# Optimization experiments

Measured on AMD Instinct MI355X. Metric: run time of the kernel, lower is better.

## Reference

```python
import math
import jax, jax.numpy as jnp
import numpy as np

NQ = 4   # n_qubits
NL = 2   # n_layers
H = 16   # num_heads


def _apply_gate(state, gate, q, batched):
    """Apply a 1-qubit gate on wire q to batched state [N, 2**NQ]."""
    n = state.shape[0]
    left, right = 2 ** q, 2 ** (NQ - 1 - q)
    s = state.reshape(n, left, 2, right)
    eq = 'nab,nlbr->nlar' if batched else 'ab,nlbr->nlar'
    return jnp.einsum(eq, gate, s).reshape(n, 2 ** NQ)


def _rot(phi, theta, omega):
    """PennyLane Rot(phi, theta, omega) = RZ(omega) RY(theta) RZ(phi), 2x2 unitary."""
    c = jnp.cos(theta / 2).astype(jnp.complex64)
    s = jnp.sin(theta / 2).astype(jnp.complex64)
    ep = jnp.exp(-0.5j * (phi + omega).astype(jnp.complex64))
    em = jnp.exp(0.5j * (phi - omega).astype(jnp.complex64))
    m00 = ep * c
    m01 = -em * s
    m10 = jnp.conj(em) * s
    m11 = jnp.conj(ep) * c
    return jnp.stack([jnp.stack([m00, m01]), jnp.stack([m10, m11])])


def _cnot01(state):
    """CNOT with control wire 0, target wire 1 on [N, 16]."""
    n = state.shape[0]
    s = state.reshape(n, 2, 2, 2 ** (NQ - 2))
    s = jnp.stack([s[:, 0], s[:, 1, ::-1]], axis=1)
    return s.reshape(n, 2 ** NQ)


def _quantum_block(inputs, params):
    """Analytic state-vector simulation of the PennyLane circuit.

    inputs: [N, NQ] rotation angles (AngleEmbedding, default RX).
    params: [NL, NQ, 3] Rot parameters.
    Returns [N, NQ] Pauli-Z expectation values.
    """
    n = inputs.shape[0]
    state = jnp.zeros((n, 2 ** NQ), jnp.complex64).at[:, 0].set(1.0)
    # AngleEmbedding: RX(inputs[:, q]) on wire q
    for q in range(NQ):
        a = inputs[:, q] * 0.5
        c = jnp.cos(a).astype(jnp.complex64)
        s = (-1j) * jnp.sin(a).astype(jnp.complex64)
        gate = jnp.stack([jnp.stack([c, s], -1), jnp.stack([s, c], -1)], -2)  # [N,2,2]
        state = _apply_gate(state, gate, q, batched=True)
    # Variational layers
    for l in range(NL):
        for q in range(NQ):
            g = _rot(params[l, q, 0], params[l, q, 1], params[l, q, 2])
            state = _apply_gate(state, g, q, batched=False)
        state = _cnot01(state)
    probs = (jnp.abs(state) ** 2).reshape(n, 2, 2, 2, 2)
    z = jnp.array([1.0, -1.0], probs.dtype)
    letters = 'abcd'
    evs = [jnp.einsum(f'nabcd,{letters[i]}->n', probs, z) for i in range(NQ)]
    return jnp.stack(evs, axis=-1)


def reference(x, params, w_q, w_k, w_v, w_o):
    B, S, E = x.shape
    dk = E // H

    def proj(w):
        return (x @ w.T).reshape(B, S, H, dk).transpose(0, 2, 1, 3)  # [B,H,S,dk]

    q, k, v = proj(w_q), proj(w_k), proj(w_v)

    def inject(t):
        ang = t[..., :NQ].reshape(-1, NQ)
        ev = _quantum_block(ang, params).reshape(B, H, S, NQ).astype(t.dtype)
        return t.at[..., :NQ].set(ev)

    q, k, v = inject(q), inject(k), inject(v)
    scores = jnp.einsum('bhqd,bhkd->bhqk', q, k) / math.sqrt(dk)
    attn = jax.nn.softmax(scores, axis=-1)
    out = jnp.einsum('bhqk,bhkd->bhqd', attn, v)
    out = out.transpose(0, 2, 1, 3).reshape(B, S, E)
    return out @ w_o.T


def setup_inputs() -> dict:
    key = jax.random.key(0)
    ks = jax.random.split(key, 6)
    B, S, E = 2, 2048, 1024
    scale = 1.0 / math.sqrt(E)
    return {
        'x': jax.random.normal(ks[0], (B, S, E), jnp.float32),
        'params': jax.random.normal(ks[1], (NL, NQ, 3), jnp.float32),
        'w_q': jax.random.normal(ks[2], (E, E), jnp.float32) * scale,
        'w_k': jax.random.normal(ks[3], (E, E), jnp.float32) * scale,
        'w_v': jax.random.normal(ks[4], (E, E), jnp.float32) * scale,
        'w_o': jax.random.normal(ks[5], (E, E), jnp.float32) * scale,
    }
```

## Files before the change

kernel.cpp:

```cpp
#include <hip/hip_runtime.h>
#include <math.h>

#define BATCH 2
#define S_LEN 2048
#define E_DIM 1024
#define NHEAD 16
#define DK 64
#define NROWS (BATCH * S_LEN)

typedef _Float16 f16x8 __attribute__((ext_vector_type(8)));
typedef _Float16 f16x4 __attribute__((ext_vector_type(4)));
typedef float    f32x4 __attribute__((ext_vector_type(4)));

__device__ __forceinline__ void glds16(_Float16* lds, const _Float16* g) {
    __builtin_amdgcn_global_load_lds(
        (const __attribute__((address_space(1))) unsigned int*)g,
        (__attribute__((address_space(3))) unsigned int*)lds,
        16, 0, 0);
}

__global__ __launch_bounds__(256) void conv_all(
    const float* __restrict__ x,  const float* __restrict__ wq,
    const float* __restrict__ wk, const float* __restrict__ wv,
    const float* __restrict__ wo,
    _Float16* __restrict__ xh,  _Float16* __restrict__ wqh,
    _Float16* __restrict__ wkh, _Float16* __restrict__ wvh,
    _Float16* __restrict__ woh) {
    const int id = blockIdx.x;
    const float* src; _Float16* dst; int lid;
    if (id < 4096)      { src = x;  dst = xh;  lid = id; }
    else if (id < 5120) { src = wq; dst = wqh; lid = id - 4096; }
    else if (id < 6144) { src = wk; dst = wkh; lid = id - 5120; }
    else if (id < 7168) { src = wv; dst = wvh; lid = id - 6144; }
    else                { src = wo; dst = woh; lid = id - 7168; }
    const int i = lid * 256 + threadIdx.x;
    float4 v = ((const float4*)src)[i];
    f16x4 h;
    h[0] = (_Float16)v.x; h[1] = (_Float16)v.y;
    h[2] = (_Float16)v.z; h[3] = (_Float16)v.w;
    ((f16x4*)dst)[i] = h;
}

__device__ __forceinline__ void gemm_body(const _Float16* __restrict__ X,
                                          const _Float16* __restrict__ W,
                                          void* __restrict__ dstv, int mode,
                                          _Float16* smem) {
    _Float16* Xs = smem;
    _Float16* Ws = smem + 128 * 64;

    const int tid  = threadIdx.x;
    const int lane = tid & 63;
    const int w    = tid >> 6;
    const int wy = w >> 1, wx = w & 1;
    const int l15 = lane & 15, quad = lane >> 4;
    const int sw  = l15 & 7;
    const int m0 = blockIdx.y * 128, c0 = blockIdx.x * 128;

    const int lrow = lane >> 3;
    const int gcol = ((lane & 7) ^ lrow) * 8;
    const _Float16* xg = X + (size_t)(m0 + w * 32 + lrow) * E_DIM + gcol;
    const _Float16* wg = W + (size_t)(c0 + w * 32 + lrow) * E_DIM + gcol;
    _Float16* xls = Xs + (w * 32) * 64;
    _Float16* wls = Ws + (w * 32) * 64;

    f32x4 acc[4][4];
#pragma unroll
    for (int i = 0; i < 4; ++i)
#pragma unroll
        for (int j = 0; j < 4; ++j) acc[i][j] = 0.f;

    for (int k0 = 0; k0 < E_DIM; k0 += 64) {
        __syncthreads();
#pragma unroll
        for (int c = 0; c < 4; ++c)
            glds16(xls + c * 512, xg + (size_t)c * 8 * E_DIM + k0);
#pragma unroll
        for (int c = 0; c < 4; ++c)
            glds16(wls + c * 512, wg + (size_t)c * 8 * E_DIM + k0);
        __syncthreads();

#pragma unroll
        for (int ks = 0; ks < 2; ++ks) {
            f16x8 af[4], bf[4];
#pragma unroll
            for (int i = 0; i < 4; ++i) {
                const int pc = ((ks * 4 + quad) ^ sw) * 8;
                af[i] = *(const f16x8*)&Xs[(wy * 64 + i * 16 + l15) * 64 + pc];
                bf[i] = *(const f16x8*)&Ws[(wx * 64 + i * 16 + l15) * 64 + pc];
            }
#pragma unroll
            for (int i = 0; i < 4; ++i)
#pragma unroll
                for (int j = 0; j < 4; ++j)
                    acc[i][j] = __builtin_amdgcn_mfma_f32_16x16x32_f16(af[i], bf[j], acc[i][j], 0, 0, 0);
        }
    }

    if (mode == 2) {
        __syncthreads();
        _Float16* Ct = smem;
#pragma unroll
        for (int i = 0; i < 4; ++i)
#pragma unroll
            for (int j = 0; j < 4; ++j) {
                const int col  = wx * 64 + j * 16 + l15;
                const int rowb = wy * 64 + i * 16 + quad * 4;
                f16x4 pk;
#pragma unroll
                for (int r = 0; r < 4; ++r) pk[r] = (_Float16)acc[i][j][r];
                *(f16x4*)&Ct[col * 136 + rowb] = pk;
            }
        __syncthreads();
        const int b  = m0 >> 11;
        const int s0 = m0 & 2047;
#pragma unroll
        for (int it = 0; it < 8; ++it) {
            const int c   = it * 256 + tid;
            const int col = c >> 4;
            const int rc  = c & 15;
            f16x8 v = *(const f16x8*)&Ct[col * 136 + rc * 8];
            const int e = c0 + col, h = e >> 6, d = e & 63;
            *(f16x8*)((_Float16*)dstv + ((size_t)((b * NHEAD + h) * DK + d)) * S_LEN + s0 + rc * 8) = v;
        }
        return;
    }

#pragma unroll
    for (int i = 0; i < 4; ++i)
#pragma unroll
        for (int j = 0; j < 4; ++j)
#pragma unroll
            for (int r = 0; r < 4; ++r) {
                const int row = m0 + wy * 64 + i * 16 + quad * 4 + r;
                const int col = c0 + wx * 64 + j * 16 + l15;
                const int b = row >> 11, s = row & 2047;
                const int h = col >> 6,  d = col & 63;
                ((_Float16*)dstv)[(((size_t)(b * NHEAD + h) * S_LEN + s) * DK) + d] =
                    (_Float16)acc[i][j][r];
            }
}

__global__ __launch_bounds__(256, 3) void gemm_qkv(
    const _Float16* __restrict__ X,
    const _Float16* __restrict__ WQ, const _Float16* __restrict__ WK,
    const _Float16* __restrict__ WV,
    _Float16* __restrict__ Qh, _Float16* __restrict__ Kh,
    _Float16* __restrict__ VTh) {
    __shared__ __align__(16) _Float16 smem[128 * 136];
    const int z = blockIdx.z;
    const _Float16* W = (z == 0) ? WQ : (z == 1) ? WK : WV;
    void* dst = (z == 0) ? (void*)Qh : (z == 1) ? (void*)Kh : (void*)VTh;
    gemm_body(X, W, dst, (z == 2) ? 2 : 1, smem);
}

__global__ __launch_bounds__(256, 2) void gemm_out2(const _Float16* __restrict__ X,
                                                    const _Float16* __restrict__ W,
                                                    float* __restrict__ dst) {
    __shared__ __align__(16) _Float16 smem[128 * 64 + 64 * 64];
    _Float16* Xs = smem;
    _Float16* Ws = smem + 128 * 64;

    const int tid  = threadIdx.x;
    const int lane = tid & 63;
    const int w    = tid >> 6;
    const int wy = w >> 1, wx = w & 1;
    const int l15 = lane & 15, quad = lane >> 4;
    const int sw  = l15 & 7;
    const int m0 = blockIdx.y * 128, c0 = blockIdx.x * 64;

    const int lrow = lane >> 3;
    const int gcol = ((lane & 7) ^ lrow) * 8;
    const _Float16* xg = X + (size_t)(m0 + w * 32 + lrow) * E_DIM + gcol;
    const _Float16* wg = W + (size_t)(c0 + w * 16 + lrow) * E_DIM + gcol;
    _Float16* xls = Xs + (w * 32) * 64;
    _Float16* wls = Ws + (w * 16) * 64;

    f32x4 acc[4][2];
#pragma unroll
    for (int i = 0; i < 4; ++i)
#pragma unroll
        for (int j = 0; j < 2; ++j) acc[i][j] = 0.f;

    for (int k0 = 0; k0 < E_DIM; k0 += 64) {
        __syncthreads();
#pragma unroll
        for (int c = 0; c < 4; ++c)
            glds16(xls + c * 512, xg + (size_t)c * 8 * E_DIM + k0);
#pragma unroll
        for (int c = 0; c < 2; ++c)
            glds16(wls + c * 512, wg + (size_t)c * 8 * E_DIM + k0);
        __syncthreads();

#pragma unroll
        for (int ks = 0; ks < 2; ++ks) {
            f16x8 af[4], bf[2];
#pragma unroll
            for (int i = 0; i < 4; ++i) {
                const int pc = ((ks * 4 + quad) ^ sw) * 8;
                af[i] = *(const f16x8*)&Xs[(wy * 64 + i * 16 + l15) * 64 + pc];
            }
#pragma unroll
            for (int j = 0; j < 2; ++j) {
                const int pc = ((ks * 4 + quad) ^ sw) * 8;
                bf[j] = *(const f16x8*)&Ws[(wx * 32 + j * 16 + l15) * 64 + pc];
            }
#pragma unroll
            for (int i = 0; i < 4; ++i)
#pragma unroll
                for (int j = 0; j < 2; ++j)
                    acc[i][j] = __builtin_amdgcn_mfma_f32_16x16x32_f16(af[i], bf[j], acc[i][j], 0, 0, 0);
        }
    }

#pragma unroll
    for (int i = 0; i < 4; ++i)
#pragma unroll
        for (int j = 0; j < 2; ++j)
#pragma unroll
            for (int r = 0; r < 4; ++r) {
                const int row = m0 + wy * 64 + i * 16 + quad * 4 + r;
                const int col = c0 + wx * 32 + j * 16 + l15;
                dst[(size_t)row * E_DIM + col] = acc[i][j][r];
            }
}

__device__ __forceinline__ void apply_gate(float ar[16], float ai[16], int stride,
                                           float g00r, float g00i, float g01r, float g01i,
                                           float g10r, float g10i, float g11r, float g11i) {
#pragma unroll
    for (int i0 = 0; i0 < 16; ++i0) {
        if (i0 & stride) continue;
        const int i1 = i0 + stride;
        const float s0r = ar[i0], s0i = ai[i0];
        const float s1r = ar[i1], s1i = ai[i1];
        ar[i0] = g00r * s0r - g00i * s0i + g01r * s1r - g01i * s1i;
        ai[i0] = g00r * s0i + g00i * s0r + g01r * s1i + g01i * s1r;
        ar[i1] = g10r * s0r - g10i * s0i + g11r * s1r - g11i * s1i;
        ai[i1] = g10r * s0i + g10i * s0r + g11r * s1i + g11i * s1r;
    }
}

__global__ __launch_bounds__(256) void quantum_inject(_Float16* __restrict__ Q,
                                                      _Float16* __restrict__ K,
                                                      _Float16* __restrict__ VT,
                                                      const float* __restrict__ params) {
    const int id = blockIdx.x * 256 + threadIdx.x;
    const int which = id >> 16;
    const int rem = id & 65535;

    float angv[4];
    _Float16* qkbase = nullptr;
    _Float16* vbase  = nullptr;
    if (which == 2) {
        const int bh = rem >> 11, s = rem & 2047;
        vbase = VT + ((size_t)bh * DK) * S_LEN + s;
#pragma unroll
        for (int d = 0; d < 4; ++d) angv[d] = (float)vbase[(size_t)d * S_LEN];
    } else {
        qkbase = (which == 0 ? Q : K) + (size_t)rem * DK;
        const f16x4 a4 = *(const f16x4*)qkbase;
#pragma unroll
        for (int d = 0; d < 4; ++d) angv[d] = (float)a4[d];
    }

    float ar[16], ai[16];
#pragma unroll
    for (int i = 0; i < 16; ++i) { ar[i] = 0.f; ai[i] = 0.f; }
    ar[0] = 1.f;

#pragma unroll
    for (int q = 0; q < 4; ++q) {
        float sh, ch;
        sincosf(0.5f * angv[q], &sh, &ch);
        apply_gate(ar, ai, 8 >> q, ch, 0.f, 0.f, -sh, 0.f, -sh, ch, 0.f);
    }

#pragma unroll
    for (int l = 0; l < 2; ++l) {
#pragma unroll
        for (int q = 0; q < 4; ++q) {
            const float* pp = params + (l * 4 + q) * 3;
            const float phi = pp[0], th = pp[1], om = pp[2];
            float st, ct, sa, ca, sb, cb;
            sincosf(0.5f * th, &st, &ct);
            sincosf(0.5f * (phi + om), &sa, &ca);
            sincosf(0.5f * (phi - om), &sb, &cb);
            apply_gate(ar, ai, 8 >> q,
                       ct * ca, -ct * sa,
                       -st * cb, -st * sb,
                       st * cb, -st * sb,
                       ct * ca, ct * sa);
        }
#pragma unroll
        for (int r = 0; r < 4; ++r) {
            float tr = ar[8 + r], ti = ai[8 + r];
            ar[8 + r] = ar[12 + r]; ai[8 + r] = ai[12 + r];
            ar[12 + r] = tr;        ai[12 + r] = ti;
        }
    }

    float ev[4] = {0.f, 0.f, 0.f, 0.f};
#pragma unroll
    for (int i = 0; i < 16; ++i) {
        const float p = ar[i] * ar[i] + ai[i] * ai[i];
        ev[0] += (i & 8) ? -p : p;
        ev[1] += (i & 4) ? -p : p;
        ev[2] += (i & 2) ? -p : p;
        ev[3] += (i & 1) ? -p : p;
    }
    if (which == 2) {
#pragma unroll
        for (int d = 0; d < 4; ++d) vbase[(size_t)d * S_LEN] = (_Float16)ev[d];
    } else {
        f16x4 o;
#pragma unroll
        for (int d = 0; d < 4; ++d) o[d] = (_Float16)ev[d];
        *(f16x4*)qkbase = o;
    }
}

__global__ __launch_bounds__(256, 3) void attn7(const _Float16* __restrict__ Q,
                                                const _Float16* __restrict__ K,
                                                const _Float16* __restrict__ VT,
                                                _Float16* __restrict__ ctx) {
    __shared__ __align__(16) _Float16 KVs[2][2][64 * 64];

    const int tid = threadIdx.x, lane = tid & 63, w = tid >> 6;
    const int l15 = lane & 15, quad = lane >> 4;
    const int sw  = l15 & 7;
    const int bh = blockIdx.y;
    const int qbase = blockIdx.x * 128 + w * 32;

    const _Float16* Qb = Q  + (size_t)bh * S_LEN * DK;
    const _Float16* Kb = K  + (size_t)bh * S_LEN * DK;
    const _Float16* Vb = VT + (size_t)bh * DK * S_LEN;

    const int lrow = lane >> 3;
    const int gcol = ((lane & 7) ^ lrow) * 8;
    const int sr0  = 32 * (w >> 1) + 8 * (lrow >> 2) + 4 * (w & 1) + (lrow & 3);
    const _Float16* kg = Kb + (size_t)sr0 * DK + gcol;
    const _Float16* vg = Vb + (size_t)(w * 16 + lrow) * S_LEN + gcol;

    f16x8 bf[2][2];
#pragma unroll
    for (int qn = 0; qn < 2; ++qn)
#pragma unroll
        for (int ks = 0; ks < 2; ++ks)
            bf[qn][ks] = *(const f16x8*)(Qb + (size_t)(qbase + qn * 16 + l15) * DK + ks * 32 + quad * 8);

    f32x4 oacc[4][2];
#pragma unroll
    for (int dt = 0; dt < 4; ++dt)
#pragma unroll
        for (int qn = 0; qn < 2; ++qn) oacc[dt][qn] = 0.f;
    float lpart[2] = {0.f, 0.f};

#pragma unroll
    for (int c = 0; c < 2; ++c) {
        glds16(&KVs[0][0][(w * 16 + c * 8) * 64], kg + (size_t)(c * 16) * DK);
        glds16(&KVs[0][1][(w * 16 + c * 8) * 64], vg + (size_t)(c * 8) * S_LEN);
    }
    __syncthreads();

    for (int t = 0; t < S_LEN / 64; ++t) {
        const int buf = t & 1;
        if (t < S_LEN / 64 - 1) {
            const int kt = (t + 1) * 64;
#pragma unroll
            for (int c = 0; c < 2; ++c) {
                glds16(&KVs[buf ^ 1][0][(w * 16 + c * 8) * 64],
                       kg + (size_t)(kt + c * 16) * DK);
                glds16(&KVs[buf ^ 1][1][(w * 16 + c * 8) * 64],
                       vg + (size_t)(c * 8) * S_LEN + kt);
            }
        }

        f16x8 af[4][2], vt[4][2];
#pragma unroll
        for (int kc = 0; kc < 4; ++kc)
#pragma unroll
            for (int ks = 0; ks < 2; ++ks)
                af[kc][ks] = *(const f16x8*)&KVs[buf][0][(kc * 16 + l15) * 64 + ((ks * 4 + quad) ^ sw) * 8];
#pragma unroll
        for (int dt = 0; dt < 4; ++dt)
#pragma unroll
            for (int kh = 0; kh < 2; ++kh)
                vt[dt][kh] = *(const f16x8*)&KVs[buf][1][(dt * 16 + l15) * 64 + ((kh * 4 + quad) ^ sw) * 8];

        f16x4 pk4s[4][2];
#pragma unroll
        for (int kc = 0; kc < 4; ++kc)
#pragma unroll
            for (int qn = 0; qn < 2; ++qn) {
                f32x4 st = 0.f;
                st = __builtin_amdgcn_mfma_f32_16x16x32_f16(af[kc][0], bf[qn][0], st, 0, 0, 0);
                st = __builtin_amdgcn_mfma_f32_16x16x32_f16(af[kc][1], bf[qn][1], st, 0, 0, 0);
                float ps = 0.f;
                f16x4 pk;
#pragma unroll
                for (int r = 0; r < 4; ++r) {
                    const float p = __builtin_amdgcn_exp2f(
                        fmaf(st[r], 0.18033688011f, -4.32808512267f));
                    ps += p;
                    pk[r] = (_Float16)p;
                }
                lpart[qn] += ps;
                pk4s[kc][qn] = pk;
            }

#pragma unroll
        for (int dt = 0; dt < 4; ++dt)
#pragma unroll
            for (int qn = 0; qn < 2; ++qn)
#pragma unroll
                for (int kh = 0; kh < 2; ++kh) {
                    const f16x8 pb = __builtin_shufflevector(
                        pk4s[2 * kh][qn], pk4s[2 * kh + 1][qn],
                        0, 1, 2, 3, 4, 5, 6, 7);
                    oacc[dt][qn] = __builtin_amdgcn_mfma_f32_16x16x32_f16(
                        vt[dt][kh], pb, oacc[dt][qn], 0, 0, 0);
                }

        __syncthreads();
    }

    float inv[2];
#pragma unroll
    for (int qn = 0; qn < 2; ++qn) {
        float l = lpart[qn];
        l += __shfl_xor(l, 16);
        l += __shfl_xor(l, 32);
        inv[qn] = 1.f / l;
    }

    _Float16* ep = &KVs[0][0][0] + w * (32 * 72);
#pragma unroll
    for (int dt = 0; dt < 4; ++dt)
#pragma unroll
        for (int qn = 0; qn < 2; ++qn) {
            f16x4 ov;
#pragma unroll
            for (int r = 0; r < 4; ++r) ov[r] = (_Float16)(oacc[dt][qn][r] * inv[qn]);
            *(f16x4*)&ep[(qn * 16 + l15) * 72 + dt * 16 + quad * 4] = ov;
        }

    const int b = bh >> 4, h = bh & 15;
#pragma unroll
    for (int i = 0; i < 4; ++i) {
        const int c = i * 64 + lane;
        const int row = c >> 3, c8 = c & 7;
        f16x8 v = *(const f16x8*)&ep[row * 72 + c8 * 8];
        *(f16x8*)(ctx + (size_t)(b * S_LEN + qbase + row) * E_DIM + h * DK + c8 * 8) = v;
    }
}

extern "C" void kernel_launch(void* const* d_in, const int* in_sizes, int n_in,
                              void* d_out, int out_size, void* d_ws, size_t ws_size,
                              hipStream_t stream) {
    const float* x      = (const float*)d_in[0];
    const float* params = (const float*)d_in[1];
    const float* w_q    = (const float*)d_in[2];
    const float* w_k    = (const float*)d_in[3];
    const float* w_v    = (const float*)d_in[4];
    const float* w_o    = (const float*)d_in[5];
    float* out = (float*)d_out;

    const size_t TENS = (size_t)NROWS * E_DIM;
    const size_t WEL  = (size_t)E_DIM * E_DIM;
    _Float16* xh  = (_Float16*)d_ws;
    _Float16* wqh = xh  + TENS;
    _Float16* wkh = wqh + WEL;
    _Float16* wvh = wkh + WEL;
    _Float16* woh = wvh + WEL;
    _Float16* Qh  = woh + WEL;
    _Float16* Kh  = Qh  + TENS;
    _Float16* VTh = Kh  + TENS;
    _Float16* CTXh= VTh + TENS;

    dim3 blk(256);

    conv_all<<<dim3(8192), blk, 0, stream>>>(x, w_q, w_k, w_v, w_o,
                                             xh, wqh, wkh, wvh, woh);

    gemm_qkv<<<dim3(E_DIM / 128, NROWS / 128, 3), blk, 0, stream>>>(
        xh, wqh, wkh, wvh, Qh, Kh, VTh);

    quantum_inject<<<dim3(768), blk, 0, stream>>>(Qh, Kh, VTh, params);

    attn7<<<dim3(S_LEN / 128, BATCH * NHEAD), blk, 0, stream>>>(Qh, Kh, VTh, CTXh);

    gemm_out2<<<dim3(E_DIM / 64, NROWS / 128), blk, 0, stream>>>(CTXh, woh, out);
}
```

Measured before the change: 197.9 us.

## Double-buffer LDS tiles in QKV and output GEMMs to overlap loads with MFMA

After: 190.3 us. -3.9%, faster.

```diff
diff --git a/kernel.cpp b/kernel.cpp
--- a/kernel.cpp
+++ b/kernel.cpp
@@ -45,9 +45,6 @@
                                           const _Float16* __restrict__ W,
                                           void* __restrict__ dstv, int mode,
                                           _Float16* smem) {
-    _Float16* Xs = smem;
-    _Float16* Ws = smem + 128 * 64;
-
     const int tid  = threadIdx.x;
     const int lane = tid & 63;
     const int w    = tid >> 6;
@@ -60,8 +57,7 @@
     const int gcol = ((lane & 7) ^ lrow) * 8;
     const _Float16* xg = X + (size_t)(m0 + w * 32 + lrow) * E_DIM + gcol;
     const _Float16* wg = W + (size_t)(c0 + w * 32 + lrow) * E_DIM + gcol;
-    _Float16* xls = Xs + (w * 32) * 64;
-    _Float16* wls = Ws + (w * 32) * 64;
+    const int woff = (w * 32) * 64;
 
     f32x4 acc[4][4];
 #pragma unroll
@@ -69,15 +65,26 @@
 #pragma unroll
         for (int j = 0; j < 4; ++j) acc[i][j] = 0.f;
 
-    for (int k0 = 0; k0 < E_DIM; k0 += 64) {
-        __syncthreads();
-#pragma unroll
-        for (int c = 0; c < 4; ++c)
-            glds16(xls + c * 512, xg + (size_t)c * 8 * E_DIM + k0);
-#pragma unroll
-        for (int c = 0; c < 4; ++c)
-            glds16(wls + c * 512, wg + (size_t)c * 8 * E_DIM + k0);
-        __syncthreads();
+#pragma unroll
+    for (int c = 0; c < 4; ++c) {
+        glds16(smem + woff + c * 512,        xg + (size_t)c * 8 * E_DIM);
+        glds16(smem + 8192 + woff + c * 512, wg + (size_t)c * 8 * E_DIM);
+    }
+    __syncthreads();
+
+    for (int t = 0; t < E_DIM / 64; ++t) {
+        const int buf = t & 1;
+        _Float16* Xs = smem + buf * 16384;
+        _Float16* Ws = Xs + 8192;
+        if (t < E_DIM / 64 - 1) {
+            _Float16* Xn = smem + (buf ^ 1) * 16384;
+            const int k0 = (t + 1) * 64;
+#pragma unroll
+            for (int c = 0; c < 4; ++c) {
+                glds16(Xn + woff + c * 512,        xg + (size_t)c * 8 * E_DIM + k0);
+                glds16(Xn + 8192 + woff + c * 512, wg + (size_t)c * 8 * E_DIM + k0);
+            }
+        }
 
 #pragma unroll
         for (int ks = 0; ks < 2; ++ks) {
@@ -94,10 +101,10 @@
                 for (int j = 0; j < 4; ++j)
                     acc[i][j] = __builtin_amdgcn_mfma_f32_16x16x32_f16(af[i], bf[j], acc[i][j], 0, 0, 0);
         }
+        __syncthreads();
     }
 
     if (mode == 2) {
-        __syncthreads();
         _Float16* Ct = smem;
 #pragma unroll
         for (int i = 0; i < 4; ++i)
@@ -140,25 +147,23 @@
             }
 }
 
-__global__ __launch_bounds__(256, 3) void gemm_qkv(
+__global__ __launch_bounds__(256, 2) void gemm_qkv(
     const _Float16* __restrict__ X,
     const _Float16* __restrict__ WQ, const _Float16* __restrict__ WK,
     const _Float16* __restrict__ WV,
     _Float16* __restrict__ Qh, _Float16* __restrict__ Kh,
     _Float16* __restrict__ VTh) {
-    __shared__ __align__(16) _Float16 smem[128 * 136];
+    __shared__ __align__(16) _Float16 smem[2 * 16384];
     const int z = blockIdx.z;
     const _Float16* W = (z == 0) ? WQ : (z == 1) ? WK : WV;
     void* dst = (z == 0) ? (void*)Qh : (z == 1) ? (void*)Kh : (void*)VTh;
     gemm_body(X, W, dst, (z == 2) ? 2 : 1, smem);
 }
 
-__global__ __launch_bounds__(256, 2) void gemm_out2(const _Float16* __restrict__ X,
+__global__ __launch_bounds__(256, 3) void gemm_out2(const _Float16* __restrict__ X,
                                                     const _Float16* __restrict__ W,
                                                     float* __restrict__ dst) {
-    __shared__ __align__(16) _Float16 smem[128 * 64 + 64 * 64];
-    _Float16* Xs = smem;
-    _Float16* Ws = smem + 128 * 64;
+    __shared__ __align__(16) _Float16 smem[2 * 12288];
 
     const int tid  = threadIdx.x;
     const int lane = tid & 63;
@@ -172,8 +177,8 @@
     const int gcol = ((lane & 7) ^ lrow) * 8;
     const _Float16* xg = X + (size_t)(m0 + w * 32 + lrow) * E_DIM + gcol;
     const _Float16* wg = W + (size_t)(c0 + w * 16 + lrow) * E_DIM + gcol;
-    _Float16* xls = Xs + (w * 32) * 64;
-    _Float16* wls = Ws + (w * 16) * 64;
+    const int xoff = (w * 32) * 64;
+    const int woff = (w * 16) * 64;
 
     f32x4 acc[4][2];
 #pragma unroll
@@ -181,15 +186,28 @@
 #pragma unroll
         for (int j = 0; j < 2; ++j) acc[i][j] = 0.f;
 
-    for (int k0 = 0; k0 < E_DIM; k0 += 64) {
-        __syncthreads();
-#pragma unroll
-        for (int c = 0; c < 4; ++c)
-            glds16(xls + c * 512, xg + (size_t)c * 8 * E_DIM + k0);
-#pragma unroll
-        for (int c = 0; c < 2; ++c)
-            glds16(wls + c * 512, wg + (size_t)c * 8 * E_DIM + k0);
-        __syncthreads();
+#pragma unroll
+    for (int c = 0; c < 4; ++c)
+        glds16(smem + xoff + c * 512, xg + (size_t)c * 8 * E_DIM);
+#pragma unroll
+    for (int c = 0; c < 2; ++c)
+        glds16(smem + 8192 + woff + c * 512, wg + (size_t)c * 8 * E_DIM);
+    __syncthreads();
+
+    for (int t = 0; t < E_DIM / 64; ++t) {
+        const int buf = t & 1;
+        _Float16* Xs = smem + buf * 12288;
+        _Float16* Ws = Xs + 8192;
+        if (t < E_DIM / 64 - 1) {
+            _Float16* Xn = smem + (buf ^ 1) * 12288;
+            const int k0 = (t + 1) * 64;
+#pragma unroll
+            for (int c = 0; c < 4; ++c)
+                glds16(Xn + xoff + c * 512, xg + (size_t)c * 8 * E_DIM + k0);
+#pragma unroll
+            for (int c = 0; c < 2; ++c)
+                glds16(Xn + 8192 + woff + c * 512, wg + (size_t)c * 8 * E_DIM + k0);
+        }
 
 #pragma unroll
         for (int ks = 0; ks < 2; ++ks) {
@@ -210,6 +228,7 @@
                 for (int j = 0; j < 2; ++j)
                     acc[i][j] = __builtin_amdgcn_mfma_f32_16x16x32_f16(af[i], bf[j], acc[i][j], 0, 0, 0);
         }
+        __syncthreads();
     }
 
 #pragma unroll
```
